# Kernel optimization log

Hardware: AMD Instinct MI355X
Metric: run time of the kernel (lower is better)

## Reference

```python
import jax, jax.numpy as jnp
import numpy as np

B, S, D, H, L, OUT = 4, 1024, 1024, 16, 6, 512
HD = D // H
EPS = 1e-5


def _positional_encoding(seq, dim):
    pos = np.arange(seq, dtype=np.float32)[:, None]          # [S,1]
    i = np.arange(0, dim, 2, dtype=np.float32)[None, :]       # even indices
    div = np.power(10000.0, 2.0 * i / dim)                    # repo's (nonstandard) exponent
    pe = np.zeros((seq, dim), dtype=np.float32)
    pe[:, 0::2] = np.sin(pos / div)
    pe[:, 1::2] = np.cos(pos / div)
    return jnp.asarray(pe)[None]                               # [1,S,D]


def _causal_mask(seq):
    r = jnp.arange(seq)
    m = jnp.where(r[None, :] > r[:, None], jnp.float32(-jnp.inf), jnp.float32(0.0))
    return m[None, None]                                       # [1,1,S,S]


def setup_inputs() -> dict:
    key = jax.random.key(0)
    ks = jax.random.split(key, 10)
    sc = 0.02
    inp = {
        'x':      jax.random.normal(ks[0], (B, S, D), jnp.float32),
        'pe':     _positional_encoding(S, D),
        'mask':   _causal_mask(S),
        'ln1_g':  jnp.ones((L, D), jnp.float32),
        'ln1_b':  jnp.zeros((L, D), jnp.float32),
        'wq':     jax.random.normal(ks[1], (L, D, D), jnp.float32) * sc,
        'wk':     jax.random.normal(ks[2], (L, D, D), jnp.float32) * sc,
        'wv':     jax.random.normal(ks[3], (L, D, D), jnp.float32) * sc,
        'wo':     jax.random.normal(ks[4], (L, D, D), jnp.float32) * sc,
        'ln2_g':  jnp.ones((L, D), jnp.float32),
        'ln2_b':  jnp.zeros((L, D), jnp.float32),
        'wf':     jax.random.normal(ks[5], (L, D, D), jnp.float32) * sc,
        'lnf_g':  jnp.ones((D,), jnp.float32),
        'lnf_b':  jnp.zeros((D,), jnp.float32),
        'w_out':  jax.random.normal(ks[6], (OUT, D), jnp.float32) * sc,
    }
    return inp


def _layer_norm(x, g, b):
    mu = jnp.mean(x, axis=-1, keepdims=True)
    var = jnp.mean(jnp.square(x - mu), axis=-1, keepdims=True)
    return (x - mu) * jax.lax.rsqrt(var + EPS) * g + b


def _split_heads(x):
    b, s, d = x.shape
    return x.reshape(b, s, H, HD).transpose(0, 2, 1, 3)  # [B,H,S,HD]


def reference(x, pe, mask, ln1_g, ln1_b, wq, wk, wv, wo, ln2_g, ln2_b, wf, lnf_g, lnf_b, w_out):
    h = x + pe
    scale = 1.0 / jnp.sqrt(jnp.float32(HD))
    for l in range(wq.shape[0]):
        h_ = _layer_norm(h, ln1_g[l], ln1_b[l])
        q = _split_heads(jnp.einsum('bsd,ed->bse', h_, wq[l]))
        k = _split_heads(jnp.einsum('bsd,ed->bse', h_, wk[l]))
        v = _split_heads(jnp.einsum('bsd,ed->bse', h_, wv[l]))
        scores = jnp.einsum('bhqd,bhkd->bhqk', q, k) * scale + mask  # [B,H,S,S]
        probs = jax.nn.softmax(scores, axis=-1)
        attn = jnp.einsum('bhqk,bhkd->bhqd', probs, v)
        attn = attn.transpose(0, 2, 1, 3).reshape(h.shape)            # combine heads
        h = h + jnp.einsum('bsd,ed->bse', attn, wo[l])
        h_ = _layer_norm(h, ln2_g[l], ln2_b[l])
        h = h + jnp.einsum('bsd,ed->bse', h_, wf[l])                  # FFN = plain linear (no activation, as in source)
    h = _layer_norm(h, lnf_g, lnf_b)
    return jnp.einsum('bsd,od->bso', h, w_out)
```

## Files before the change

### kernel.cpp

```cpp
#include <hip/hip_runtime.h>
#include <hip/hip_bf16.h>
#include <stdint.h>

#define BATCH 4
#define SEQ   1024
#define DIM   1024
#define NH    16
#define HDIM  64
#define NLAYER 6
#define NOUT  512
#define NTOK  (BATCH*SEQ)
#define LOG2E 1.44269504088896f
#define NEG_BIG (-1e30f)
#define VTS   72

using bf16 = __hip_bfloat16;
typedef __attribute__((ext_vector_type(4))) float f32x4;
typedef __attribute__((ext_vector_type(8))) short bf16x8;
typedef __attribute__((ext_vector_type(4))) short bf16x4;

typedef __attribute__((address_space(1))) void as1_void;
typedef __attribute__((address_space(3))) void as3_void;

__device__ __forceinline__ float bf2f(short u) {
  union { unsigned int i; float f; } c;
  c.i = ((unsigned int)(unsigned short)u) << 16;
  return c.f;
}

__device__ __forceinline__ short f2bs(float f) {
  bf16 h = __float2bfloat16(f);
  return *(short*)&h;
}

__device__ __forceinline__ float exp_clamped(float x) {
  return exp2f(fmaxf(x, -100.f) * LOG2E);
}

__device__ __forceinline__ float loadf(const void* p, size_t i, bool f32) {
  return f32 ? ((const float*)p)[i] : __bfloat162float(((const bf16*)p)[i]);
}

__device__ __forceinline__ void g2l16(const void* g, void* l) {
  __builtin_amdgcn_global_load_lds((const as1_void*)g, (as3_void*)l, 16, 0, 0);
}

__global__ void sniff(const unsigned int* __restrict__ w, int* __restrict__ flag) {
  const int lane = threadIdx.x;
  const unsigned int word = w[lane];
  const int e2 = (word >> 7) & 0xFF;
  const bool bf16ish = (e2 >= 0x60) && (e2 <= 0x8F);
  const unsigned long long m = __ballot(bf16ish);
  if (lane == 0) *flag = (__popcll(m) >= 48) ? 0 : 1;
}

__global__ __launch_bounds__(256) void convert_all(
    const float* __restrict__ s0, const float* __restrict__ s1,
    const float* __restrict__ s2, const float* __restrict__ s3,
    const float* __restrict__ s4, const float* __restrict__ s5,
    bf16* __restrict__ d0, bf16* __restrict__ d1, bf16* __restrict__ d2,
    bf16* __restrict__ d3, bf16* __restrict__ d4, bf16* __restrict__ d5,
    const int* __restrict__ flag) {
  if (*flag == 0) return;
  int b = blockIdx.x;
  const float* s; bf16* d;
  if      (b <  768) { s = s0; d = d0; }
  else if (b < 1536) { s = s1; d = d1; b -= 768; }
  else if (b < 2304) { s = s2; d = d2; b -= 1536; }
  else if (b < 3072) { s = s3; d = d3; b -= 2304; }
  else if (b < 3840) { s = s4; d = d4; b -= 3072; }
  else               { s = s5; d = d5; b -= 3840; }
  const size_t e0 = ((size_t)b * 1024 + threadIdx.x) * 8;
  f32x4 a[4], c[4];
#pragma unroll
  for (int i = 0; i < 4; ++i) {
    a[i] = *(const f32x4*)(s + e0 + i * 2048);
    c[i] = *(const f32x4*)(s + e0 + i * 2048 + 4);
  }
#pragma unroll
  for (int i = 0; i < 4; ++i) {
    bf16x8 o;
    o[0] = f2bs(a[i][0]); o[1] = f2bs(a[i][1]); o[2] = f2bs(a[i][2]); o[3] = f2bs(a[i][3]);
    o[4] = f2bs(c[i][0]); o[5] = f2bs(c[i][1]); o[6] = f2bs(c[i][2]); o[7] = f2bs(c[i][3]);
    *(bf16x8*)(d + e0 + i * 2048) = o;
  }
}

__device__ __forceinline__ bf16x8 rd_frag(const short* panel, int row, int quad) {
  const int g  = row >> 1;
  const int cc = (((row & 1) << 2) | quad) ^ (g & 7);
  return *(const bf16x8*)(panel + g * 64 + cc * 8);
}

template<int EPI>
__device__ __forceinline__ void gemm_body(const bf16* __restrict__ A,
                                          const bf16* __restrict__ W,
                                          void* __restrict__ C,
                                          const int* __restrict__ flag,
                                          int N, int m0, int n0) {
  __shared__ __align__(16) short lA[8192];
  __shared__ __align__(16) short lB[8192];
  const int tid  = threadIdx.x;
  const int wave = tid >> 6;
  const int lane = tid & 63;
  const int quad = lane >> 4;
  const int l16  = lane & 15;
  const int wm = (wave >> 1) * 64;
  const int wn = (wave & 1) * 64;
  const int K = DIM;

  const int c3   = (lane & 7) ^ (lane >> 3);
  const int sq   = (c3 & 3) * 8;
  const int rsub = ((lane >> 3) << 1) | (c3 >> 2);
  const int ldsW = wave * 512;

  bool f32out = false;
  if (EPI == 2) f32out = (*flag != 0);

  f32x4 acc[4][4];
#pragma unroll
  for (int i = 0; i < 4; ++i)
#pragma unroll
    for (int j = 0; j < 4; ++j) acc[i][j] = (f32x4){0.f, 0.f, 0.f, 0.f};

  for (int k0 = 0; k0 < K; k0 += 64) {
    __syncthreads();
#pragma unroll
    for (int kc = 0; kc < 2; ++kc)
#pragma unroll
      for (int c = 0; c < 2; ++c) {
        const int row = c * 64 + wave * 16 + rsub;
        g2l16(A + (size_t)(m0 + row) * K + k0 + kc * 32 + sq,
              lA + kc * 4096 + c * 2048 + ldsW);
        g2l16(W + (size_t)(n0 + row) * K + k0 + kc * 32 + sq,
              lB + kc * 4096 + c * 2048 + ldsW);
      }
    __builtin_amdgcn_s_waitcnt(0);
    __syncthreads();

#pragma unroll
    for (int kc = 0; kc < 2; ++kc) {
      const short* pA = lA + kc * 4096;
      const short* pB = lB + kc * 4096;
      bf16x8 af[4], bfr[4];
#pragma unroll
      for (int i = 0; i < 4; ++i) {
        af[i]  = rd_frag(pA, wm + i * 16 + l16, quad);
        bfr[i] = rd_frag(pB, wn + i * 16 + l16, quad);
      }
#pragma unroll
      for (int i = 0; i < 4; ++i)
#pragma unroll
        for (int j = 0; j < 4; ++j)
          acc[i][j] = __builtin_amdgcn_mfma_f32_16x16x32_bf16(af[i], bfr[j], acc[i][j], 0, 0, 0);
    }
  }

#pragma unroll
  for (int i = 0; i < 4; ++i) {
    const int rowb = m0 + wm + i * 16 + quad * 4;
#pragma unroll
    for (int j = 0; j < 4; ++j) {
      const int col = n0 + wn + j * 16 + l16;
#pragma unroll
      for (int r = 0; r < 4; ++r) {
        const size_t idx = (size_t)(rowb + r) * N + col;
        const float v = acc[i][j][r];
        if (EPI == 0) ((bf16*)C)[idx] = __float2bfloat16(v);
        else { if (f32out) ((float*)C)[idx] = v; else ((bf16*)C)[idx] = __float2bfloat16(v); }
      }
    }
  }
}

__global__ __launch_bounds__(256) void gemm_qkv(const bf16* __restrict__ A,
                                                const bf16* __restrict__ cq,
                                                const bf16* __restrict__ ck,
                                                const bf16* __restrict__ cvv,
                                                const bf16* __restrict__ oq,
                                                const bf16* __restrict__ ok,
                                                const bf16* __restrict__ ov,
                                                bf16* __restrict__ q,
                                                bf16* __restrict__ k,
                                                bf16* __restrict__ v,
                                                const int* __restrict__ flag) {
  const int gx = blockIdx.x;
  const int sel = gx >> 3;
  const int n0 = (gx & 7) * 128;
  const bool f32 = (*flag != 0);
  const bf16* W = (sel == 0) ? (f32 ? cq : oq)
                 : (sel == 1) ? (f32 ? ck : ok)
                              : (f32 ? cvv : ov);
  bf16* C = (sel == 0) ? q : (sel == 1 ? k : v);
  gemm_body<0>(A, W, C, nullptr, DIM, blockIdx.y * 128, n0);
}

template<int EPI>
__device__ __forceinline__ void gemm64_body(const bf16* __restrict__ A,
                                            const bf16* __restrict__ W,
                                            void* __restrict__ C,
                                            const int* __restrict__ flag,
                                            int N, int m0, int n0) {
  __shared__ __align__(16) short lA[4096];
  __shared__ __align__(16) short lB[8192];
  const int tid  = threadIdx.x;
  const int wave = tid >> 6;
  const int lane = tid & 63;
  const int quad = lane >> 4;
  const int l16  = lane & 15;
  const int wm = (wave >> 1) * 32;
  const int wn = (wave & 1) * 64;
  const int K = DIM;

  const int c3   = (lane & 7) ^ (lane >> 3);
  const int sq   = (c3 & 3) * 8;
  const int rsub = ((lane >> 3) << 1) | (c3 >> 2);
  const int ldsW = wave * 512;

  bool f32out = false;
  if (EPI == 2) f32out = (*flag != 0);

  f32x4 acc[2][4];
#pragma unroll
  for (int i = 0; i < 2; ++i)
#pragma unroll
    for (int j = 0; j < 4; ++j) acc[i][j] = (f32x4){0.f, 0.f, 0.f, 0.f};

  for (int k0 = 0; k0 < K; k0 += 64) {
    __syncthreads();
#pragma unroll
    for (int kc = 0; kc < 2; ++kc) {
      const int arow = wave * 16 + rsub;
      g2l16(A + (size_t)(m0 + arow) * K + k0 + kc * 32 + sq,
            lA + kc * 2048 + ldsW);
#pragma unroll
      for (int c = 0; c < 2; ++c) {
        const int brow = c * 64 + wave * 16 + rsub;
        g2l16(W + (size_t)(n0 + brow) * K + k0 + kc * 32 + sq,
              lB + kc * 4096 + c * 2048 + ldsW);
      }
    }
    __builtin_amdgcn_s_waitcnt(0);
    __syncthreads();

#pragma unroll
    for (int kc = 0; kc < 2; ++kc) {
      const short* pA = lA + kc * 2048;
      const short* pB = lB + kc * 4096;
      bf16x8 af[2], bfr[4];
#pragma unroll
      for (int i = 0; i < 2; ++i)
        af[i] = rd_frag(pA, wm + i * 16 + l16, quad);
#pragma unroll
      for (int j = 0; j < 4; ++j)
        bfr[j] = rd_frag(pB, wn + j * 16 + l16, quad);
#pragma unroll
      for (int i = 0; i < 2; ++i)
#pragma unroll
        for (int j = 0; j < 4; ++j)
          acc[i][j] = __builtin_amdgcn_mfma_f32_16x16x32_bf16(af[i], bfr[j], acc[i][j], 0, 0, 0);
    }
  }

#pragma unroll
  for (int i = 0; i < 2; ++i) {
    const int rowb = m0 + wm + i * 16 + quad * 4;
#pragma unroll
    for (int j = 0; j < 4; ++j) {
      const int col = n0 + wn + j * 16 + l16;
#pragma unroll
      for (int r = 0; r < 4; ++r) {
        const size_t idx = (size_t)(rowb + r) * N + col;
        const float v = acc[i][j][r];
        if (EPI == 0) ((float*)C)[idx] += v;
        else { if (f32out) ((float*)C)[idx] = v; else ((bf16*)C)[idx] = __float2bfloat16(v); }
      }
    }
  }
}

__global__ __launch_bounds__(256) void gemm_add(const bf16* __restrict__ A,
                                                const bf16* __restrict__ Wc,
                                                const bf16* __restrict__ Wo,
                                                const int* __restrict__ flag,
                                                float* __restrict__ C) {
  const bf16* W = (*flag != 0) ? Wc : Wo;
  gemm64_body<0>(A, W, C, nullptr, DIM, blockIdx.y * 64, blockIdx.x * 128);
}

__global__ __launch_bounds__(256) void gemm_out(const bf16* __restrict__ A,
                                                const bf16* __restrict__ Wc,
                                                const bf16* __restrict__ Wo,
                                                void* __restrict__ C,
                                                const int* __restrict__ flag) {
  const bf16* W = (*flag != 0) ? Wc : Wo;
  gemm64_body<2>(A, W, C, flag, NOUT, blockIdx.y * 64, blockIdx.x * 128);
}

__global__ __launch_bounds__(256) void add_pe(const void* __restrict__ x,
                                              const void* __restrict__ pe,
                                              float* __restrict__ h,
                                              const int* __restrict__ flag) {
  const bool f32 = (*flag != 0);
  const size_t i = ((size_t)blockIdx.x * 256 + threadIdx.x) * 4;
  const size_t p = i & (SEQ * DIM - 1);
  f32x4 r;
  if (f32) {
    const f32x4 xv = *(const f32x4*)((const float*)x + i);
    const f32x4 pv = *(const f32x4*)((const float*)pe + p);
#pragma unroll
    for (int e = 0; e < 4; ++e) r[e] = xv[e] + pv[e];
  } else {
    const bf16x4 xv = *(const bf16x4*)((const bf16*)x + i);
    const bf16x4 pv = *(const bf16x4*)((const bf16*)pe + p);
#pragma unroll
    for (int e = 0; e < 4; ++e) r[e] = bf2f(xv[e]) + bf2f(pv[e]);
  }
  *(f32x4*)(h + i) = r;
}

__global__ __launch_bounds__(256) void layernorm(const float* __restrict__ x,
                                                 const void* __restrict__ g,
                                                 const void* __restrict__ b,
                                                 int loff,
                                                 bf16* __restrict__ y,
                                                 const int* __restrict__ flag) {
  const bool f32 = (*flag != 0);
  const int row = blockIdx.x;
  const int tid = threadIdx.x;
  const int wave = tid >> 6;
  const float* xr = x + (size_t)row * DIM;
  __shared__ float red[8];

  float v[4];
  float s = 0.f;
#pragma unroll
  for (int i = 0; i < 4; ++i) { v[i] = xr[tid + 256 * i]; s += v[i]; }
#pragma unroll
  for (int off = 32; off >= 1; off >>= 1) s += __shfl_xor(s, off);
  if ((tid & 63) == 0) red[wave] = s;
  __syncthreads();
  const float mu = (red[0] + red[1] + red[2] + red[3]) * (1.f / DIM);

  float vs = 0.f;
#pragma unroll
  for (int i = 0; i < 4; ++i) { const float d = v[i] - mu; vs += d * d; }
#pragma unroll
  for (int off = 32; off >= 1; off >>= 1) vs += __shfl_xor(vs, off);
  if ((tid & 63) == 0) red[4 + wave] = vs;
  __syncthreads();
  const float var = (red[4] + red[5] + red[6] + red[7]) * (1.f / DIM);
  const float rs = rsqrtf(var + 1e-5f);

#pragma unroll
  for (int i = 0; i < 4; ++i) {
    const int d = tid + 256 * i;
    const float gv = loadf(g, (size_t)loff + d, f32);
    const float bv = loadf(b, (size_t)loff + d, f32);
    y[(size_t)row * DIM + d] = __float2bfloat16((v[i] - mu) * rs * gv + bv);
  }
}

__global__ __launch_bounds__(256, 2) void attn_flash(const bf16* __restrict__ q,
                                                     const bf16* __restrict__ k,
                                                     const bf16* __restrict__ v,
                                                     bf16* __restrict__ o) {
  __shared__ __align__(16) short lK[2 * 64 * 64];
  __shared__ __align__(16) short lVT[2 * 64 * VTS];
  __shared__ __align__(16) short lP[4 * 16 * VTS];

  const int idx = blockIdx.x;
  const int qt = (SEQ / 64 - 1) - (idx >> 6);
  const int bh = idx & 63;
  const int hh = bh & (NH - 1);
  const int bb = bh >> 4;
  const int q0 = qt * 64;

  const int tid = threadIdx.x;
  const int wave = tid >> 6;
  const int lane = tid & 63;
  const int quad = lane >> 4;
  const int l16 = lane & 15;

  const size_t base = (size_t)bb * SEQ * DIM + hh * HDIM;
  const int qlo = q0 + wave * 16;

  bf16x8 qf[2];
  {
    const bf16* qr = q + base + (size_t)(qlo + l16) * DIM;
#pragma unroll
    for (int kc = 0; kc < 2; ++kc) {
      bf16x8 t = *(const bf16x8*)(qr + kc * 32 + quad * 8);
      bf16x8 sq;
#pragma unroll
      for (int e = 0; e < 8; ++e) sq[e] = f2bs(bf2f(t[e]) * 0.125f);
      qf[kc] = sq;
    }
  }

  float l_acc[4] = {0.f, 0.f, 0.f, 0.f};
  f32x4 oacc[4];
#pragma unroll
  for (int nb = 0; nb < 4; ++nb) oacc[nb] = (f32x4){0.f, 0.f, 0.f, 0.f};

  short* lPw = lP + wave * 16 * VTS;
  const int nt = qt + 1;

  for (int t0 = 0; t0 < nt; t0 += 2) {
    __syncthreads();

    {
      const int r8 = lane >> 3;
      const int cc = (lane & 7) ^ r8;
#pragma unroll
      for (int h2 = 0; h2 < 2; ++h2) {
        if (t0 + h2 < nt) {
          const int kbase = (t0 + h2) * 64;
#pragma unroll
          for (int c = 0; c < 2; ++c) {
            const int row = wave * 16 + c * 8 + r8;
            g2l16(k + base + (size_t)(kbase + row) * DIM + cc * 8,
                  lK + h2 * 4096 + (wave * 16 + c * 8) * 64);
          }
        }
      }
    }

    bf16x8 vch[2][2];
#pragma unroll
    for (int h2 = 0; h2 < 2; ++h2) {
      if (t0 + h2 < nt) {
        const int kbase = (t0 + h2) * 64;
#pragma unroll
        for (int c2 = 0; c2 < 2; ++c2) {
          const int cid = tid + c2 * 256;
          const int kk = cid >> 3;
          const int d0 = (cid & 7) * 8;
          vch[h2][c2] = *(const bf16x8*)(v + base + (size_t)(kbase + kk) * DIM + d0);
        }
      }
    }
#pragma unroll
    for (int h2 = 0; h2 < 2; ++h2) {
      if (t0 + h2 < nt) {
#pragma unroll
        for (int c2 = 0; c2 < 2; ++c2) {
          const int cid = tid + c2 * 256;
          const int kk = cid >> 3;
          const int d0 = (cid & 7) * 8;
#pragma unroll
          for (int e = 0; e < 8; ++e) {
            const int d = d0 + e;
            const int kks = kk ^ (((d >> 3) & 7) << 3);
            lVT[h2 * 64 * VTS + d * VTS + kks] = vch[h2][c2][e];
          }
        }
      }
    }
    __builtin_amdgcn_s_waitcnt(0);
    __syncthreads();

#pragma unroll
    for (int h2 = 0; h2 < 2; ++h2) {
      const int t = t0 + h2;
      if (t < nt) {
        const int kbase = t * 64;
        const short* lKh = lK + h2 * 4096;
        const short* lVh = lVT + h2 * 64 * VTS;

        f32x4 s[4];
#pragma unroll
        for (int nb = 0; nb < 4; ++nb) {
          f32x4 acc = (f32x4){0.f, 0.f, 0.f, 0.f};
          const int n = nb * 16 + l16;
#pragma unroll
          for (int kc = 0; kc < 2; ++kc) {
            const int cidx = (kc * 4 + quad) ^ (n & 7);
            bf16x8 kf = *(const bf16x8*)(lKh + n * 64 + cidx * 8);
            acc = __builtin_amdgcn_mfma_f32_16x16x32_bf16(qf[kc], kf, acc, 0, 0, 0);
          }
          s[nb] = acc;
        }

        if (kbase + 63 > qlo) {
#pragma unroll
          for (int nb = 0; nb < 4; ++nb) {
            const int j = kbase + nb * 16 + l16;
#pragma unroll
            for (int r = 0; r < 4; ++r)
              if (j > qlo + quad * 4 + r) s[nb][r] = NEG_BIG;
          }
        }

#pragma unroll
        for (int nb = 0; nb < 4; ++nb) {
#pragma unroll
          for (int r = 0; r < 4; ++r) {
            const float p = exp_clamped(s[nb][r]);
            l_acc[r] += p;
            lPw[(quad * 4 + r) * VTS + nb * 16 + l16] = f2bs(p);
          }
        }

        __builtin_amdgcn_s_waitcnt(0);
        bf16x8 pf[2];
#pragma unroll
        for (int kc = 0; kc < 2; ++kc)
          pf[kc] = *(const bf16x8*)(lPw + l16 * VTS + kc * 32 + quad * 8);

#pragma unroll
        for (int nb = 0; nb < 4; ++nb) {
          const int n = nb * 16 + l16;
          const int swz = ((n >> 3) & 7) << 3;
#pragma unroll
          for (int kc = 0; kc < 2; ++kc) {
            const int kchunk = (kc * 32 + quad * 8) ^ swz;
            bf16x8 vf = *(const bf16x8*)(lVh + n * VTS + kchunk);
            oacc[nb] = __builtin_amdgcn_mfma_f32_16x16x32_bf16(pf[kc], vf, oacc[nb], 0, 0, 0);
          }
        }
      }
    }
  }

  float linv[4];
#pragma unroll
  for (int r = 0; r < 4; ++r) {
    float ts = l_acc[r];
#pragma unroll
    for (int off = 8; off >= 1; off >>= 1) ts += __shfl_xor(ts, off);
    linv[r] = 1.f / ts;
  }
#pragma unroll
  for (int nb = 0; nb < 4; ++nb)
#pragma unroll
    for (int r = 0; r < 4; ++r) {
      const int qrow = q0 + wave * 16 + quad * 4 + r;
      o[base + (size_t)qrow * DIM + nb * 16 + l16] =
          __float2bfloat16(oacc[nb][r] * linv[r]);
    }
}

extern "C" void kernel_launch(void* const* d_in, const int* in_sizes, int n_in,
                              void* d_out, int out_size, void* d_ws, size_t ws_size,
                              hipStream_t stream) {
  const void* x    = d_in[0];
  const void* pe   = d_in[1];
  const void* ln1g = d_in[3];
  const void* ln1b = d_in[4];
  const void* wq   = d_in[5];
  const void* wk   = d_in[6];
  const void* wv   = d_in[7];
  const void* wo   = d_in[8];
  const void* ln2g = d_in[9];
  const void* ln2b = d_in[10];
  const void* wf   = d_in[11];
  const void* lnfg = d_in[12];
  const void* lnfb = d_in[13];
  const void* wout = d_in[14];

  const size_t MB = 1u << 20;
  char* ws = (char*)d_ws;
  int*  flag = (int*)ws;
  bf16* wqc  = (bf16*)(ws + 1 * MB);
  bf16* wkc  = (bf16*)(ws + 13 * MB);
  bf16* wvc  = (bf16*)(ws + 25 * MB);
  bf16* woc  = (bf16*)(ws + 37 * MB);
  bf16* wfc  = (bf16*)(ws + 49 * MB);
  bf16* woutc= (bf16*)(ws + 61 * MB);
  float* h   = (float*)(ws + 62 * MB);
  bf16* hn   = (bf16*)(ws + 78 * MB);
  bf16* qb   = (bf16*)(ws + 86 * MB);
  bf16* kb   = (bf16*)(ws + 94 * MB);
  bf16* vb   = (bf16*)(ws + 102 * MB);
  bf16* ab   = hn;

  sniff<<<1, 64, 0, stream>>>((const unsigned int*)wq, flag);

  convert_all<<<3904, 256, 0, stream>>>(
      (const float*)wq, (const float*)wk, (const float*)wv,
      (const float*)wo, (const float*)wf, (const float*)wout,
      wqc, wkc, wvc, woc, wfc, woutc, flag);

  add_pe<<<NTOK * DIM / (256 * 4), 256, 0, stream>>>(x, pe, h, flag);

  for (int l = 0; l < NLAYER; ++l) {
    const size_t woff = (size_t)l << 20;
    const int poff = l * DIM;
    layernorm<<<NTOK, 256, 0, stream>>>(h, ln1g, ln1b, poff, hn, flag);
    gemm_qkv<<<dim3(24, 32), 256, 0, stream>>>(
        hn, wqc + woff, wkc + woff, wvc + woff,
        (const bf16*)wq + woff, (const bf16*)wk + woff, (const bf16*)wv + woff,
        qb, kb, vb, flag);
    attn_flash<<<dim3(BATCH * NH * (SEQ / 64)), 256, 0, stream>>>(qb, kb, vb, ab);
    gemm_add<<<dim3(8, 64), 256, 0, stream>>>(ab, woc + woff,
                                              (const bf16*)wo + woff, flag, h);
    layernorm<<<NTOK, 256, 0, stream>>>(h, ln2g, ln2b, poff, hn, flag);
    gemm_add<<<dim3(8, 64), 256, 0, stream>>>(hn, wfc + woff,
                                              (const bf16*)wf + woff, flag, h);
  }

  layernorm<<<NTOK, 256, 0, stream>>>(h, lnfg, lnfb, 0, hn, flag);
  gemm_out<<<dim3(4, 64), 256, 0, stream>>>(hn, woutc, (const bf16*)wout,
                                            d_out, flag);
}
```

Baseline: 906.9 us.

## Double attention query tile to 128 rows and fuse PE add with first layernorm

The flash attention kernel now processes 128 query rows per block, 32 per wave in two 16-row groups. Each K/V tile loaded into LDS is reused across twice as many queries, halving K/V global traffic and sync overhead per query. This costs more registers, halves the block count (512 blocks), and the diagonal tiles do more masked work. Separately, the positional-encoding add is fused with the layer-0 layernorm into one kernel, removing one launch and one pass over h.

```diff
diff --git a/kernel.cpp b/kernel.cpp
--- a/kernel.cpp
+++ b/kernel.cpp
@@ -297,26 +297,53 @@
   gemm64_body<2>(A, W, C, flag, NOUT, blockIdx.y * 64, blockIdx.x * 128);
 }
 
-__global__ __launch_bounds__(256) void add_pe(const void* __restrict__ x,
-                                              const void* __restrict__ pe,
-                                              float* __restrict__ h,
-                                              const int* __restrict__ flag) {
+__global__ __launch_bounds__(256) void addpe_ln(const void* __restrict__ x,
+                                                const void* __restrict__ pe,
+                                                const void* __restrict__ g,
+                                                const void* __restrict__ b,
+                                                float* __restrict__ h,
+                                                bf16* __restrict__ y,
+                                                const int* __restrict__ flag) {
   const bool f32 = (*flag != 0);
-  const size_t i = ((size_t)blockIdx.x * 256 + threadIdx.x) * 4;
-  const size_t p = i & (SEQ * DIM - 1);
-  f32x4 r;
-  if (f32) {
-    const f32x4 xv = *(const f32x4*)((const float*)x + i);
-    const f32x4 pv = *(const f32x4*)((const float*)pe + p);
-#pragma unroll
-    for (int e = 0; e < 4; ++e) r[e] = xv[e] + pv[e];
-  } else {
-    const bf16x4 xv = *(const bf16x4*)((const bf16*)x + i);
-    const bf16x4 pv = *(const bf16x4*)((const bf16*)pe + p);
-#pragma unroll
-    for (int e = 0; e < 4; ++e) r[e] = bf2f(xv[e]) + bf2f(pv[e]);
-  }
-  *(f32x4*)(h + i) = r;
+  const int row = blockIdx.x;
+  const int tid = threadIdx.x;
+  const int wave = tid >> 6;
+  const size_t xoff = (size_t)row * DIM;
+  const size_t poff = (size_t)(row & (SEQ - 1)) * DIM;
+  __shared__ float red[8];
+
+  float v[4];
+  float s = 0.f;
+#pragma unroll
+  for (int i = 0; i < 4; ++i) {
+    const int d = tid + 256 * i;
+    v[i] = loadf(x, xoff + d, f32) + loadf(pe, poff + d, f32);
+    h[xoff + d] = v[i];
+    s += v[i];
+  }
+#pragma unroll
+  for (int off = 32; off >= 1; off >>= 1) s += __shfl_xor(s, off);
+  if ((tid & 63) == 0) red[wave] = s;
+  __syncthreads();
+  const float mu = (red[0] + red[1] + red[2] + red[3]) * (1.f / DIM);
+
+  float vs = 0.f;
+#pragma unroll
+  for (int i = 0; i < 4; ++i) { const float d = v[i] - mu; vs += d * d; }
+#pragma unroll
+  for (int off = 32; off >= 1; off >>= 1) vs += __shfl_xor(vs, off);
+  if ((tid & 63) == 0) red[4 + wave] = vs;
+  __syncthreads();
+  const float var = (red[4] + red[5] + red[6] + red[7]) * (1.f / DIM);
+  const float rs = rsqrtf(var + 1e-5f);
+
+#pragma unroll
+  for (int i = 0; i < 4; ++i) {
+    const int d = tid + 256 * i;
+    const float gv = loadf(g, (size_t)d, f32);
+    const float bv = loadf(b, (size_t)d, f32);
+    y[xoff + d] = __float2bfloat16((v[i] - mu) * rs * gv + bv);
+  }
 }
 
 __global__ __launch_bounds__(256) void layernorm(const float* __restrict__ x,
@@ -367,14 +394,14 @@
                                                      bf16* __restrict__ o) {
   __shared__ __align__(16) short lK[2 * 64 * 64];
   __shared__ __align__(16) short lVT[2 * 64 * VTS];
-  __shared__ __align__(16) short lP[4 * 16 * VTS];
+  __shared__ __align__(16) short lP[4 * 32 * VTS];
 
   const int idx = blockIdx.x;
-  const int qt = (SEQ / 64 - 1) - (idx >> 6);
+  const int qt = (SEQ / 128 - 1) - (idx >> 6);
   const int bh = idx & 63;
   const int hh = bh & (NH - 1);
   const int bb = bh >> 4;
-  const int q0 = qt * 64;
+  const int q0 = qt * 128;
 
   const int tid = threadIdx.x;
   const int wave = tid >> 6;
@@ -383,28 +410,34 @@
   const int l16 = lane & 15;
 
   const size_t base = (size_t)bb * SEQ * DIM + hh * HDIM;
-  const int qlo = q0 + wave * 16;
-
-  bf16x8 qf[2];
-  {
-    const bf16* qr = q + base + (size_t)(qlo + l16) * DIM;
+  const int qlo = q0 + wave * 32;
+
+  bf16x8 qf[2][2];
+#pragma unroll
+  for (int rg = 0; rg < 2; ++rg) {
+    const bf16* qr = q + base + (size_t)(qlo + rg * 16 + l16) * DIM;
 #pragma unroll
     for (int kc = 0; kc < 2; ++kc) {
       bf16x8 t = *(const bf16x8*)(qr + kc * 32 + quad * 8);
       bf16x8 sq;
 #pragma unroll
       for (int e = 0; e < 8; ++e) sq[e] = f2bs(bf2f(t[e]) * 0.125f);
-      qf[kc] = sq;
-    }
-  }
-
-  float l_acc[4] = {0.f, 0.f, 0.f, 0.f};
-  f32x4 oacc[4];
-#pragma unroll
-  for (int nb = 0; nb < 4; ++nb) oacc[nb] = (f32x4){0.f, 0.f, 0.f, 0.f};
-
-  short* lPw = lP + wave * 16 * VTS;
-  const int nt = qt + 1;
+      qf[rg][kc] = sq;
+    }
+  }
+
+  float l_acc[2][4];
+  f32x4 oacc[2][4];
+#pragma unroll
+  for (int rg = 0; rg < 2; ++rg)
+#pragma unroll
+    for (int nb = 0; nb < 4; ++nb) {
+      oacc[rg][nb] = (f32x4){0.f, 0.f, 0.f, 0.f};
+      l_acc[rg][nb] = 0.f;
+    }
+
+  short* lPw = lP + wave * 32 * VTS;
+  const int nt = 2 * qt + 2;
 
   for (int t0 = 0; t0 < nt; t0 += 2) {
     __syncthreads();
@@ -414,131 +447,135 @@
       const int cc = (lane & 7) ^ r8;
 #pragma unroll
       for (int h2 = 0; h2 < 2; ++h2) {
-        if (t0 + h2 < nt) {
-          const int kbase = (t0 + h2) * 64;
-#pragma unroll
-          for (int c = 0; c < 2; ++c) {
-            const int row = wave * 16 + c * 8 + r8;
-            g2l16(k + base + (size_t)(kbase + row) * DIM + cc * 8,
-                  lK + h2 * 4096 + (wave * 16 + c * 8) * 64);
+        const int kbase = (t0 + h2) * 64;
+#pragma unroll
+        for (int c = 0; c < 2; ++c) {
+          const int row = wave * 16 + c * 8 + r8;
+          g2l16(k + base + (size_t)(kbase + row) * DIM + cc * 8,
+                lK + h2 * 4096 + (wave * 16 + c * 8) * 64);
+        }
+      }
+    }
+
+    bf16x8 vch[2][2];
+#pragma unroll
+    for (int h2 = 0; h2 < 2; ++h2) {
+      const int kbase = (t0 + h2) * 64;
+#pragma unroll
+      for (int c2 = 0; c2 < 2; ++c2) {
+        const int cid = tid + c2 * 256;
+        const int kk = cid >> 3;
+        const int d0 = (cid & 7) * 8;
+        vch[h2][c2] = *(const bf16x8*)(v + base + (size_t)(kbase + kk) * DIM + d0);
+      }
+    }
+#pragma unroll
+    for (int h2 = 0; h2 < 2; ++h2) {
+#pragma unroll
+      for (int c2 = 0; c2 < 2; ++c2) {
+        const int cid = tid + c2 * 256;
+        const int kk = cid >> 3;
+        const int d0 = (cid & 7) * 8;
+#pragma unroll
+        for (int e = 0; e < 8; ++e) {
+          const int d = d0 + e;
+          const int kks = kk ^ (((d >> 3) & 7) << 3);
+          lVT[h2 * 64 * VTS + d * VTS + kks] = vch[h2][c2][e];
+        }
+      }
+    }
+    __builtin_amdgcn_s_waitcnt(0);
+    __syncthreads();
+
+#pragma unroll
+    for (int h2 = 0; h2 < 2; ++h2) {
+      const int kbase = (t0 + h2) * 64;
+      const short* lKh = lK + h2 * 4096;
+      const short* lVh = lVT + h2 * 64 * VTS;
+
+      f32x4 sS[2][4];
+#pragma unroll
+      for (int nb = 0; nb < 4; ++nb) {
+        f32x4 a0 = (f32x4){0.f, 0.f, 0.f, 0.f};
+        f32x4 a1 = (f32x4){0.f, 0.f, 0.f, 0.f};
+        const int n = nb * 16 + l16;
+#pragma unroll
+        for (int kc = 0; kc < 2; ++kc) {
+          const int cidx = (kc * 4 + quad) ^ (n & 7);
+          bf16x8 kf = *(const bf16x8*)(lKh + n * 64 + cidx * 8);
+          a0 = __builtin_amdgcn_mfma_f32_16x16x32_bf16(qf[0][kc], kf, a0, 0, 0, 0);
+          a1 = __builtin_amdgcn_mfma_f32_16x16x32_bf16(qf[1][kc], kf, a1, 0, 0, 0);
+        }
+        sS[0][nb] = a0; sS[1][nb] = a1;
+      }
+
+#pragma unroll
+      for (int rg = 0; rg < 2; ++rg) {
+        const int qlor = qlo + rg * 16;
+        if (kbase + 63 > qlor) {
+#pragma unroll
+          for (int nb = 0; nb < 4; ++nb) {
+            const int j = kbase + nb * 16 + l16;
+#pragma unroll
+            for (int r = 0; r < 4; ++r)
+              if (j > qlor + quad * 4 + r) sS[rg][nb][r] = NEG_BIG;
           }
         }
       }
-    }
-
-    bf16x8 vch[2][2];
-#pragma unroll
-    for (int h2 = 0; h2 < 2; ++h2) {
-      if (t0 + h2 < nt) {
-        const int kbase = (t0 + h2) * 64;
-#pragma unroll
-        for (int c2 = 0; c2 < 2; ++c2) {
-          const int cid = tid + c2 * 256;
-          const int kk = cid >> 3;
-          const int d0 = (cid & 7) * 8;
-          vch[h2][c2] = *(const bf16x8*)(v + base + (size_t)(kbase + kk) * DIM + d0);
+
+#pragma unroll
+      for (int rg = 0; rg < 2; ++rg)
+#pragma unroll
+        for (int nb = 0; nb < 4; ++nb)
+#pragma unroll
+          for (int r = 0; r < 4; ++r) {
+            const float p = exp_clamped(sS[rg][nb][r]);
+            l_acc[rg][r] += p;
+            lPw[(rg * 16 + quad * 4 + r) * VTS + nb * 16 + l16] = f2bs(p);
+          }
+
+      __builtin_amdgcn_s_waitcnt(0);
+      bf16x8 pf[2][2];
+#pragma unroll
+      for (int rg = 0; rg < 2; ++rg)
+#pragma unroll
+        for (int kc = 0; kc < 2; ++kc)
+          pf[rg][kc] = *(const bf16x8*)(lPw + (rg * 16 + l16) * VTS + kc * 32 + quad * 8);
+
+#pragma unroll
+      for (int nb = 0; nb < 4; ++nb) {
+        const int n = nb * 16 + l16;
+        const int swz = ((n >> 3) & 7) << 3;
+#pragma unroll
+        for (int kc = 0; kc < 2; ++kc) {
+          const int kchunk = (kc * 32 + quad * 8) ^ swz;
+          bf16x8 vf = *(const bf16x8*)(lVh + n * VTS + kchunk);
+          oacc[0][nb] = __builtin_amdgcn_mfma_f32_16x16x32_bf16(pf[0][kc], vf, oacc[0][nb], 0, 0, 0);
+          oacc[1][nb] = __builtin_amdgcn_mfma_f32_16x16x32_bf16(pf[1][kc], vf, oacc[1][nb], 0, 0, 0);
         }
       }
     }
-#pragma unroll
-    for (int h2 = 0; h2 < 2; ++h2) {
-      if (t0 + h2 < nt) {
-#pragma unroll
-        for (int c2 = 0; c2 < 2; ++c2) {
-          const int cid = tid + c2 * 256;
-          const int kk = cid >> 3;
-          const int d0 = (cid & 7) * 8;
-#pragma unroll
-          for (int e = 0; e < 8; ++e) {
-            const int d = d0 + e;
-            const int kks = kk ^ (((d >> 3) & 7) << 3);
-            lVT[h2 * 64 * VTS + d * VTS + kks] = vch[h2][c2][e];
-          }
-        }
-      }
-    }
-    __builtin_amdgcn_s_waitcnt(0);
-    __syncthreads();
-
-#pragma unroll
-    for (int h2 = 0; h2 < 2; ++h2) {
-      const int t = t0 + h2;
-      if (t < nt) {
-        const int kbase = t * 64;
-        const short* lKh = lK + h2 * 4096;
-        const short* lVh = lVT + h2 * 64 * VTS;
-
-        f32x4 s[4];
-#pragma unroll
-        for (int nb = 0; nb < 4; ++nb) {
-          f32x4 acc = (f32x4){0.f, 0.f, 0.f, 0.f};
-          const int n = nb * 16 + l16;
-#pragma unroll
-          for (int kc = 0; kc < 2; ++kc) {
-            const int cidx = (kc * 4 + quad) ^ (n & 7);
-            bf16x8 kf = *(const bf16x8*)(lKh + n * 64 + cidx * 8);
-            acc = __builtin_amdgcn_mfma_f32_16x16x32_bf16(qf[kc], kf, acc, 0, 0, 0);
-          }
-          s[nb] = acc;
-        }
-
-        if (kbase + 63 > qlo) {
-#pragma unroll
-          for (int nb = 0; nb < 4; ++nb) {
-            const int j = kbase + nb * 16 + l16;
-#pragma unroll
-            for (int r = 0; r < 4; ++r)
-              if (j > qlo + quad * 4 + r) s[nb][r] = NEG_BIG;
-          }
-        }
-
-#pragma unroll
-        for (int nb = 0; nb < 4; ++nb) {
-#pragma unroll
-          for (int r = 0; r < 4; ++r) {
-            const float p = exp_clamped(s[nb][r]);
-            l_acc[r] += p;
-            lPw[(quad * 4 + r) * VTS + nb * 16 + l16] = f2bs(p);
-          }
-        }
-
-        __builtin_amdgcn_s_waitcnt(0);
-        bf16x8 pf[2];
-#pragma unroll
-        for (int kc = 0; kc < 2; ++kc)
-          pf[kc] = *(const bf16x8*)(lPw + l16 * VTS + kc * 32 + quad * 8);
-
-#pragma unroll
-        for (int nb = 0; nb < 4; ++nb) {
-          const int n = nb * 16 + l16;
-          const int swz = ((n >> 3) & 7) << 3;
-#pragma unroll
-          for (int kc = 0; kc < 2; ++kc) {
-            const int kchunk = (kc * 32 + quad * 8) ^ swz;
-            bf16x8 vf = *(const bf16x8*)(lVh + n * VTS + kchunk);
-            oacc[nb] = __builtin_amdgcn_mfma_f32_16x16x32_bf16(pf[kc], vf, oacc[nb], 0, 0, 0);
-          }
-        }
-      }
-    }
-  }
-
-  float linv[4];
-#pragma unroll
-  for (int r = 0; r < 4; ++r) {
-    float ts = l_acc[r];
-#pragma unroll
-    for (int off = 8; off >= 1; off >>= 1) ts += __shfl_xor(ts, off);
-    linv[r] = 1.f / ts;
-  }
-#pragma unroll
-  for (int nb = 0; nb < 4; ++nb)
+  }
+
+#pragma unroll
+  for (int rg = 0; rg < 2; ++rg) {
+    float linv[4];
 #pragma unroll
     for (int r = 0; r < 4; ++r) {
-      const int qrow = q0 + wave * 16 + quad * 4 + r;
-      o[base + (size_t)qrow * DIM + nb * 16 + l16] =
-          __float2bfloat16(oacc[nb][r] * linv[r]);
-    }
+      float ts = l_acc[rg][r];
+#pragma unroll
+      for (int off = 8; off >= 1; off >>= 1) ts += __shfl_xor(ts, off);
+      linv[r] = 1.f / ts;
+    }
+#pragma unroll
+    for (int nb = 0; nb < 4; ++nb)
+#pragma unroll
+      for (int r = 0; r < 4; ++r) {
+        const int qrow = qlo + rg * 16 + quad * 4 + r;
+        o[base + (size_t)qrow * DIM + nb * 16 + l16] =
+            __float2bfloat16(oacc[rg][nb][r] * linv[r]);
+      }
+  }
 }
 
 extern "C" void kernel_launch(void* const* d_in, const int* in_sizes, int n_in,
@@ -582,17 +619,18 @@
       (const float*)wo, (const float*)wf, (const float*)wout,
       wqc, wkc, wvc, woc, wfc, woutc, flag);
 
-  add_pe<<<NTOK * DIM / (256 * 4), 256, 0, stream>>>(x, pe, h, flag);
+  addpe_ln<<<NTOK, 256, 0, stream>>>(x, pe, ln1g, ln1b, h, hn, flag);
 
   for (int l = 0; l < NLAYER; ++l) {
     const size_t woff = (size_t)l << 20;
     const int poff = l * DIM;
-    layernorm<<<NTOK, 256, 0, stream>>>(h, ln1g, ln1b, poff, hn, flag);
+    if (l > 0)
+      layernorm<<<NTOK, 256, 0, stream>>>(h, ln1g, ln1b, poff, hn, flag);
     gemm_qkv<<<dim3(24, 32), 256, 0, stream>>>(
         hn, wqc + woff, wkc + woff, wvc + woff,
         (const bf16*)wq + woff, (const bf16*)wk + woff, (const bf16*)wv + woff,
         qb, kb, vb, flag);
-    attn_flash<<<dim3(BATCH * NH * (SEQ / 64)), 256, 0, stream>>>(qb, kb, vb, ab);
+    attn_flash<<<dim3(BATCH * NH * (SEQ / 128)), 256, 0, stream>>>(qb, kb, vb, ab);
     gemm_add<<<dim3(8, 64), 256, 0, stream>>>(ab, woc + woff,
                                               (const bf16*)wo + woff, flag, h);
     layernorm<<<NTOK, 256, 0, stream>>>(h, ln2g, ln2b, poff, hn, flag);
```

Result: slower. 952.2 us (+5.0%).
